# Kernel optimization log

Hardware: AMD Instinct MI355X
Metric: run time of the kernel (lower is better)

Reference implementation:

```python
import jax, jax.numpy as jnp
import numpy as np

H = 16   # heads
DK = 64  # d_model // heads
D = 1024 # d_model


def _linear_heads(x, W, b):
    # x: (bs, n, D) -> (bs, H, n, DK)
    y = x @ W.T + b
    bs, n, _ = y.shape
    return y.reshape(bs, n, H, DK).transpose(0, 2, 1, 3)


def setup_inputs() -> dict:
    key = jax.random.key(0)
    ks = jax.random.split(key, 16)
    s = 0.02
    inp = {
        "w_feat": jax.random.normal(ks[0], (4, 128, D), jnp.float32),
        "v_feat": jax.random.normal(ks[1], (4, 1024, D), jnp.float32),
        "Ww1": jax.random.normal(ks[2], (D, D), jnp.float32) * s,
        "bw1": jnp.zeros((D,), jnp.float32),
        "Wv1": jax.random.normal(ks[3], (D, D), jnp.float32) * s,
        "bv1": jnp.zeros((D,), jnp.float32),
        "Wv2": jax.random.normal(ks[4], (D, D), jnp.float32) * s,
        "bv2": jnp.zeros((D,), jnp.float32),
        "Wv3": jax.random.normal(ks[5], (D, D), jnp.float32) * s,
        "bv3": jnp.zeros((D,), jnp.float32),
        "Wv4": jax.random.normal(ks[6], (D, D), jnp.float32) * s,
        "bv4": jnp.zeros((D,), jnp.float32),
        "Wout": jax.random.normal(ks[7], (D, D), jnp.float32) * s,
        "bout": jnp.zeros((D,), jnp.float32),
    }
    return inp


def reference(w_feat, v_feat, Ww1, bw1, Wv1, bv1, Wv2, bv2, Wv3, bv3, Wv4, bv4, Wout, bout):
    bs = w_feat.shape[0]
    w1 = _linear_heads(w_feat, Ww1, bw1)  # (bs,H,n_w,DK)
    v1 = _linear_heads(v_feat, Wv1, bv1)  # (bs,H,n_v,DK)
    v2 = _linear_heads(v_feat, Wv2, bv2)
    v3 = _linear_heads(v_feat, Wv3, bv3)
    v4 = _linear_heads(v_feat, Wv4, bv4)

    # cross path: softmax over n_v of (w1 @ v3^T), summed over n_w -> (bs,H,n_v)
    cross = jax.nn.softmax(jnp.einsum('bhwd,bhvd->bhwv', w1, v3), axis=-1).sum(-2)
    # self path: v1 @ v2^T -> (bs,H,n_v,n_v), plus broadcast cross bias
    scores = jnp.einsum('bhid,bhjd->bhij', v1, v2) + cross[:, :, None, :]
    scores = jax.nn.softmax(scores, axis=-1)  # dropout is identity at eval
    ctx = jnp.einsum('bhij,bhjd->bhid', scores, v4)  # (bs,H,n_v,DK)
    concat = ctx.transpose(0, 2, 1, 3).reshape(bs, -1, D)
    return concat @ Wout.T + bout
```

## Files before the change

kernel.cpp:

```cpp
#include <hip/hip_runtime.h>

typedef __attribute__((ext_vector_type(8))) short short8;
typedef __attribute__((ext_vector_type(4))) float f32x4;

__device__ __forceinline__ unsigned short f2bf(float f) {
  unsigned int x = __float_as_uint(f);
  x += 0x7fffu + ((x >> 16) & 1u);
  return (unsigned short)(x >> 16);
}

__device__ __forceinline__ void gload_lds16(const void* g, void* l) {
  __builtin_amdgcn_global_load_lds((const __attribute__((address_space(1))) unsigned int*)g,
                                   (__attribute__((address_space(3))) unsigned int*)l, 16, 0, 0);
}

__global__ void cvt_f2b(const float* __restrict__ s, unsigned short* __restrict__ d, int n) {
  int i = (blockIdx.x * 256 + threadIdx.x) * 4;
  if (i < n) {
    float4 v = *(const float4*)(s + i);
    ushort4 o;
    o.x = f2bf(v.x); o.y = f2bf(v.y); o.z = f2bf(v.z); o.w = f2bf(v.w);
    *(ushort4*)(d + i) = o;
  }
}

__global__ void gather_bias(const float* __restrict__ b0, const float* __restrict__ b1,
                            const float* __restrict__ b2, const float* __restrict__ b3,
                            float* __restrict__ out) {
  int i = blockIdx.x * 256 + threadIdx.x;
  const float* src = (i < 1024) ? b0 : (i < 2048) ? b1 : (i < 3072) ? b2 : b3;
  out[i] = src[i & 1023];
}

__global__ void zero_f32(float* __restrict__ p, int n4) {
  int i = blockIdx.x * 256 + threadIdx.x;
  if (i < n4) *(float4*)(p + i * 4) = float4{0.f, 0.f, 0.f, 0.f};
}

template<int MODE, int BM, int BN, int WM, int WN>
__global__ __launch_bounds__(WM * WN * 64, 2) void gemm_pipe(
    const unsigned short* __restrict__ X, const unsigned short* __restrict__ Wt,
    const float* __restrict__ bias, void* __restrict__ o0, void* __restrict__ o1,
    void* __restrict__ o2, void* __restrict__ o3, int nnShift) {
  constexpr int T = WM * WN * 64;
  constexpr int WAVES = WM * WN;
  constexpr int MR = BM / WM / 16;
  constexpr int NR = BN / WN / 16;
  constexpr int MH = MR / 2;
  constexpr int AI = BM * 8 / T;
  constexpr int BI = BN * 8 / T;
  constexpr int NT = 1024 / 64;

  __shared__ unsigned short As[2][BM][64];
  __shared__ unsigned short Bs[2][BN][64];

  const int tid = threadIdx.x, lane = tid & 63, wv = tid >> 6;
  const int wm = wv % WM, wn = wv / WM;
  const int wMb = wm * (BM / WM), wNb = wn * (BN / WN);
  const int rowbase = blockIdx.x * BM, colbase = blockIdx.y * BN;
  const int rq = lane >> 4, cq = lane & 15;

  f32x4 acc[MR][NR] = {};

  auto stage = [&](int s, int kt) {
#pragma unroll
    for (int j = 0; j < AI; ++j) {
      int cb = (j * WAVES + wv) * 64;
      int row = (cb + lane) >> 3;
      int srcc = (lane & 7) ^ (row & 7);
      gload_lds16(X + (size_t)(rowbase + row) * 1024 + kt * 64 + srcc * 8,
                  &As[s][cb >> 3][0]);
    }
#pragma unroll
    for (int j = 0; j < BI; ++j) {
      int cb = (j * WAVES + wv) * 64;
      int row = (cb + lane) >> 3;
      int srcc = (lane & 7) ^ (row & 7);
      gload_lds16(Wt + (size_t)(colbase + row) * 1024 + kt * 64 + srcc * 8,
                  &Bs[s][cb >> 3][0]);
    }
  };

  auto ktile = [&](int t, bool last) {
    if (last) asm volatile("s_waitcnt vmcnt(0)" ::: "memory");
    else      asm volatile("s_waitcnt vmcnt(8)" ::: "memory");
    __builtin_amdgcn_s_barrier();
    asm volatile("" ::: "memory");
    const int s = t & 1;
    short8 bf[NR][2];
#pragma unroll
    for (int jf = 0; jf < NR; ++jf)
#pragma unroll
      for (int kk = 0; kk < 2; ++kk) {
        int row = wNb + jf * 16 + cq;
        int pc = (kk * 4 + rq) ^ (cq & 7);
        bf[jf][kk] = *(const short8*)(&Bs[s][row][pc * 8]);
      }
#pragma unroll
    for (int mh = 0; mh < 2; ++mh) {
      short8 af[MH][2];
#pragma unroll
      for (int i = 0; i < MH; ++i)
#pragma unroll
        for (int kk = 0; kk < 2; ++kk) {
          int row = wMb + (mh * MH + i) * 16 + cq;
          int pc = (kk * 4 + rq) ^ (cq & 7);
          af[i][kk] = *(const short8*)(&As[s][row][pc * 8]);
        }
      __builtin_amdgcn_s_setprio(1);
#pragma unroll
      for (int i = 0; i < MH; ++i)
#pragma unroll
        for (int jf = 0; jf < NR; ++jf)
#pragma unroll
          for (int kk = 0; kk < 2; ++kk)
            acc[mh * MH + i][jf] = __builtin_amdgcn_mfma_f32_16x16x32_bf16(
                af[i][kk], bf[jf][kk], acc[mh * MH + i][jf], 0, 0, 0);
      __builtin_amdgcn_s_setprio(0);
    }
    asm volatile("" ::: "memory");
    __builtin_amdgcn_s_barrier();
    asm volatile("" ::: "memory");
    if (t + 2 < NT) stage(s, t + 2);
  };

  stage(0, 0);
  stage(1, 1);
  for (int t = 0; t < NT - 1; ++t) ktile(t, false);
  ktile(NT - 1, true);

#pragma unroll
  for (int m = 0; m < MR; ++m)
#pragma unroll
    for (int n = 0; n < NR; ++n)
#pragma unroll
      for (int r = 0; r < 4; ++r) {
        int grow = rowbase + wMb + m * 16 + rq * 4 + r;
        int gcol = colbase + wNb + n * 16 + cq;
        float val = acc[m][n][r] + bias[gcol];
        if (MODE == 2) {
          ((float*)o0)[(size_t)grow * 1024 + gcol] = val;
        } else if (MODE == 0) {
          int bb = grow >> nnShift;
          int nr = grow & ((1 << nnShift) - 1);
          int hh = gcol >> 6, dd = gcol & 63;
          ((unsigned short*)o0)[((((size_t)bb * 16 + hh) << nnShift) + nr) * 64 + dd] = f2bf(val);
        } else {
          int which = gcol >> 10;
          int lcol = gcol & 1023;
          int bb = grow >> 10, nr = grow & 1023;
          int hh = lcol >> 6, dd = lcol & 63;
          void* op = (which == 0) ? o0 : (which == 1) ? o1 : (which == 2) ? o2 : o3;
          if (which < 3)
            ((unsigned short*)op)[((((size_t)bb * 16 + hh) << 10) + nr) * 64 + dd] = f2bf(val);
          else
            ((unsigned short*)op)[(((size_t)bb * 16 + hh) * 64 + dd) * 1024 + nr] = f2bf(val);
        }
      }
}

__global__ __launch_bounds__(256) void cross_kernel(const unsigned short* __restrict__ w1,
                                                    const unsigned short* __restrict__ v3,
                                                    float* __restrict__ cross) {
  __shared__ float cbuf[4][1024];
  const int tid = threadIdx.x, lane = tid & 63, wv = tid >> 6;
  const int rq = lane >> 4, cq = lane & 15;
  for (int i = tid; i < 4096; i += 256) ((float*)cbuf)[i] = 0.f;
  __syncthreads();
  const int bh = blockIdx.x >> 1, half = blockIdx.x & 1;
  const unsigned short* w1h = w1 + (size_t)bh * 128 * 64;
  const unsigned short* v3h = v3 + (size_t)bh * 1024 * 64;
  const int w0 = half * 64 + wv * 16;
  short8 a_w[2];
#pragma unroll
  for (int kk = 0; kk < 2; ++kk)
    a_w[kk] = *(const short8*)(w1h + (size_t)(w0 + cq) * 64 + kk * 32 + rq * 8);
  float mrow[4], lrow[4];
#pragma unroll
  for (int r = 0; r < 4; ++r) { mrow[r] = -3e38f; lrow[r] = 0.f; }
  for (int jt = 0; jt < 1024; jt += 64) {
    f32x4 s[4] = {};
#pragma unroll
    for (int n = 0; n < 4; ++n) {
      short8 bk[2];
#pragma unroll
      for (int kk = 0; kk < 2; ++kk)
        bk[kk] = *(const short8*)(v3h + (size_t)(jt + n * 16 + cq) * 64 + kk * 32 + rq * 8);
#pragma unroll
      for (int kk = 0; kk < 2; ++kk)
        s[n] = __builtin_amdgcn_mfma_f32_16x16x32_bf16(a_w[kk], bk[kk], s[n], 0, 0, 0);
    }
    float tm[4], ps[4];
#pragma unroll
    for (int r = 0; r < 4; ++r)
      tm[r] = fmaxf(fmaxf(s[0][r], s[1][r]), fmaxf(s[2][r], s[3][r]));
    for (int off = 1; off < 16; off <<= 1)
#pragma unroll
      for (int r = 0; r < 4; ++r) tm[r] = fmaxf(tm[r], __shfl_xor(tm[r], off));
#pragma unroll
    for (int r = 0; r < 4; ++r) {
      float mn = fmaxf(mrow[r], tm[r]);
      float al = __expf(mrow[r] - mn);
      mrow[r] = mn;
      float p = 0.f;
#pragma unroll
      for (int n = 0; n < 4; ++n) p += __expf(s[n][r] - mn);
      ps[r] = p;
      lrow[r] *= al;
    }
    for (int off = 1; off < 16; off <<= 1)
#pragma unroll
      for (int r = 0; r < 4; ++r) ps[r] += __shfl_xor(ps[r], off);
#pragma unroll
    for (int r = 0; r < 4; ++r) lrow[r] += ps[r];
  }
  float rl[4];
#pragma unroll
  for (int r = 0; r < 4; ++r) rl[r] = 1.f / lrow[r];
  for (int jt = 0; jt < 1024; jt += 64) {
    f32x4 s[4] = {};
#pragma unroll
    for (int n = 0; n < 4; ++n) {
      short8 bk[2];
#pragma unroll
      for (int kk = 0; kk < 2; ++kk)
        bk[kk] = *(const short8*)(v3h + (size_t)(jt + n * 16 + cq) * 64 + kk * 32 + rq * 8);
#pragma unroll
      for (int kk = 0; kk < 2; ++kk)
        s[n] = __builtin_amdgcn_mfma_f32_16x16x32_bf16(a_w[kk], bk[kk], s[n], 0, 0, 0);
    }
    float colsum[4] = {0.f, 0.f, 0.f, 0.f};
#pragma unroll
    for (int n = 0; n < 4; ++n)
#pragma unroll
      for (int r = 0; r < 4; ++r)
        colsum[n] += __expf(s[n][r] - mrow[r]) * rl[r];
#pragma unroll
    for (int n = 0; n < 4; ++n) {
      colsum[n] += __shfl_xor(colsum[n], 16);
      colsum[n] += __shfl_xor(colsum[n], 32);
    }
    if (lane < 16) {
#pragma unroll
      for (int n = 0; n < 4; ++n) cbuf[wv][jt + n * 16 + lane] += colsum[n];
    }
  }
  __syncthreads();
  for (int j = tid; j < 1024; j += 256)
    atomicAdd(&cross[(size_t)bh * 1024 + j], cbuf[0][j] + cbuf[1][j] + cbuf[2][j] + cbuf[3][j]);
}

__global__ __launch_bounds__(256) void attn_kernel(const unsigned short* __restrict__ v1,
                                                   const unsigned short* __restrict__ v2,
                                                   const unsigned short* __restrict__ v4t,
                                                   const float* __restrict__ cross,
                                                   unsigned short* __restrict__ ctx) {
  __shared__ unsigned short Kt[2][64][64];
  __shared__ unsigned short Vt[2][64][64];
  __shared__ unsigned short Pbuf[4][16][64];
  const int bid = ((blockIdx.x & 7) << 7) | (blockIdx.x >> 3);
  const int bh = bid >> 4, ib = bid & 15;
  const int b = bh >> 4, h = bh & 15;
  const int tid = threadIdx.x, lane = tid & 63, wv = tid >> 6;
  const int rq = lane >> 4, cq = lane & 15;
  const unsigned short* v1h = v1 + (size_t)bh * 1024 * 64;
  const unsigned short* v2h = v2 + (size_t)bh * 1024 * 64;
  const unsigned short* v4h = v4t + (size_t)bh * 64 * 1024;
  const float* ch = cross + (size_t)bh * 1024;
  const int i0 = ib * 64 + wv * 16;
  const int sr = lane >> 3;
  const int sc = ((lane & 7) ^ sr) * 8;
  short8 b_q[2];
#pragma unroll
  for (int kk = 0; kk < 2; ++kk)
    b_q[kk] = *(const short8*)(v1h + (size_t)(i0 + cq) * 64 + kk * 32 + rq * 8);
  float m = -3e38f, lsum = 0.f;
  f32x4 o[4] = {};

#pragma unroll
  for (int p = 0; p < 2; ++p) {
    int r = wv * 8 + p * 32 + sr;
    gload_lds16(v2h + (size_t)r * 64 + sc, &Kt[0][wv * 8 + p * 32][0]);
    gload_lds16(v4h + (size_t)r * 1024 + sc, &Vt[0][wv * 8 + p * 32][0]);
  }
  __syncthreads();

  for (int t = 0; t < 16; ++t) {
    const int cur = t & 1;
    const int jt = t * 64;
    if (t < 15) {
#pragma unroll
      for (int p = 0; p < 2; ++p) {
        int r = wv * 8 + p * 32 + sr;
        gload_lds16(v2h + (size_t)(jt + 64 + r) * 64 + sc, &Kt[cur ^ 1][wv * 8 + p * 32][0]);
        gload_lds16(v4h + (size_t)r * 1024 + jt + 64 + sc, &Vt[cur ^ 1][wv * 8 + p * 32][0]);
      }
    }
    f32x4 s[4] = {};
#pragma unroll
    for (int mp = 0; mp < 4; ++mp) {
      const int row = mp * 16 + cq;
      const char* base = (const char*)&Kt[cur][row][0];
#pragma unroll
      for (int kk = 0; kk < 2; ++kk) {
        short8 ak = *(const short8*)(base + ((((kk << 2) | rq) ^ (cq & 7)) << 4));
        s[mp] = __builtin_amdgcn_mfma_f32_16x16x32_bf16(ak, b_q[kk], s[mp], 0, 0, 0);
      }
    }
#pragma unroll
    for (int mp = 0; mp < 4; ++mp) {
      float4 cj = *(const float4*)(ch + jt + mp * 16 + rq * 4);
      s[mp][0] += cj.x; s[mp][1] += cj.y; s[mp][2] += cj.z; s[mp][3] += cj.w;
    }
    float tm = s[0][0];
#pragma unroll
    for (int mp = 0; mp < 4; ++mp)
#pragma unroll
      for (int r = 0; r < 4; ++r) tm = fmaxf(tm, s[mp][r]);
    tm = fmaxf(tm, __shfl_xor(tm, 16));
    tm = fmaxf(tm, __shfl_xor(tm, 32));
    float mn = fmaxf(m, tm);
    float alpha = __expf(m - mn);
    m = mn;
    float ps = 0.f;
#pragma unroll
    for (int mp = 0; mp < 4; ++mp)
#pragma unroll
      for (int r = 0; r < 4; ++r) {
        float p = __expf(s[mp][r] - mn);
        s[mp][r] = p;
        ps += p;
      }
    ps += __shfl_xor(ps, 16);
    ps += __shfl_xor(ps, 32);
    lsum = lsum * alpha + ps;
    {
      char* pb = (char*)&Pbuf[wv][cq][0];
      const int sw = (cq & 7) << 4;
#pragma unroll
      for (int mp = 0; mp < 4; ++mp) {
        ushort4 pw;
        pw.x = f2bf(s[mp][0]); pw.y = f2bf(s[mp][1]);
        pw.z = f2bf(s[mp][2]); pw.w = f2bf(s[mp][3]);
        *(ushort4*)(pb + ((mp * 32 + rq * 8) ^ sw)) = pw;
      }
    }
    short8 a_p[2];
    {
      const char* pb = (const char*)&Pbuf[wv][cq][0];
      const int sw = (cq & 7) << 4;
#pragma unroll
      for (int kk = 0; kk < 2; ++kk)
        a_p[kk] = *(const short8*)(pb + ((kk * 64 + rq * 16) ^ sw));
    }
    float al[4];
#pragma unroll
    for (int r = 0; r < 4; ++r) al[r] = __shfl(alpha, rq * 4 + r);
#pragma unroll
    for (int n = 0; n < 4; ++n)
#pragma unroll
      for (int r = 0; r < 4; ++r) o[n][r] *= al[r];
#pragma unroll
    for (int n = 0; n < 4; ++n) {
      const int row = n * 16 + cq;
      const char* base = (const char*)&Vt[cur][row][0];
#pragma unroll
      for (int kk = 0; kk < 2; ++kk) {
        short8 bv = *(const short8*)(base + ((((kk << 2) | rq) ^ (cq & 7)) << 4));
        o[n] = __builtin_amdgcn_mfma_f32_16x16x32_bf16(a_p[kk], bv, o[n], 0, 0, 0);
      }
    }
    __syncthreads();
  }
  float li[4];
#pragma unroll
  for (int r = 0; r < 4; ++r) li[r] = __shfl(lsum, rq * 4 + r);
#pragma unroll
  for (int n = 0; n < 4; ++n)
#pragma unroll
    for (int r = 0; r < 4; ++r) {
      float val = o[n][r] / li[r];
      int row = i0 + rq * 4 + r;
      int col = h * 64 + n * 16 + cq;
      ctx[((size_t)b * 1024 + row) * 1024 + col] = f2bf(val);
    }
}

extern "C" void kernel_launch(void* const* d_in, const int* in_sizes, int n_in,
                              void* d_out, int out_size, void* d_ws, size_t ws_size,
                              hipStream_t stream) {
  const int bs = in_sizes[0] / (128 * 1024);
  char* w = (char*)d_ws;
  size_t off = 0;
  auto alloc = [&](size_t bytes) -> void* {
    void* p = w + off;
    off += (bytes + 255) & ~(size_t)255;
    return p;
  };
  unsigned short* wfeat_b = (unsigned short*)alloc((size_t)bs * 128 * 1024 * 2);
  unsigned short* vfeat_b = (unsigned short*)alloc((size_t)bs * 1024 * 1024 * 2);
  unsigned short* Ww1b = (unsigned short*)alloc((size_t)1024 * 1024 * 2);
  unsigned short* Wv1b = (unsigned short*)alloc((size_t)1024 * 1024 * 2);
  unsigned short* Wv2b = (unsigned short*)alloc((size_t)1024 * 1024 * 2);
  unsigned short* Wv3b = (unsigned short*)alloc((size_t)1024 * 1024 * 2);
  unsigned short* Wv4b = (unsigned short*)alloc((size_t)1024 * 1024 * 2);
  unsigned short* Woutb = (unsigned short*)alloc((size_t)1024 * 1024 * 2);
  unsigned short* w1b = (unsigned short*)alloc((size_t)bs * 16 * 128 * 64 * 2);
  unsigned short* v1b = (unsigned short*)alloc((size_t)bs * 16 * 1024 * 64 * 2);
  unsigned short* v2b = (unsigned short*)alloc((size_t)bs * 16 * 1024 * 64 * 2);
  unsigned short* v3b = (unsigned short*)alloc((size_t)bs * 16 * 1024 * 64 * 2);
  unsigned short* v4tb = (unsigned short*)alloc((size_t)bs * 16 * 64 * 1024 * 2);
  unsigned short* ctxb = (unsigned short*)alloc((size_t)bs * 1024 * 1024 * 2);
  float* crossb = (float*)alloc((size_t)bs * 16 * 1024 * 4);
  float* biascat = (float*)alloc((size_t)4096 * 4);

  auto cvt = [&](const void* src, unsigned short* dst, int n) {
    cvt_f2b<<<(n / 4 + 255) / 256, 256, 0, stream>>>((const float*)src, dst, n);
  };
  cvt(d_in[0], wfeat_b, bs * 128 * 1024);
  cvt(d_in[1], vfeat_b, bs * 1024 * 1024);
  cvt(d_in[2], Ww1b, 1024 * 1024);
  cvt(d_in[4], Wv1b, 1024 * 1024);
  cvt(d_in[6], Wv2b, 1024 * 1024);
  cvt(d_in[8], Wv3b, 1024 * 1024);
  cvt(d_in[10], Wv4b, 1024 * 1024);
  cvt(d_in[12], Woutb, 1024 * 1024);
  gather_bias<<<16, 256, 0, stream>>>((const float*)d_in[5], (const float*)d_in[7],
                                      (const float*)d_in[9], (const float*)d_in[11], biascat);
  zero_f32<<<64, 256, 0, stream>>>(crossb, bs * 16 * 1024 / 4);

  gemm_pipe<0, 128, 128, 2, 2><<<dim3(4, 8), 256, 0, stream>>>(
      wfeat_b, Ww1b, (const float*)d_in[3], w1b, nullptr, nullptr, nullptr, 7);
  gemm_pipe<3, 256, 256, 2, 4><<<dim3(16, 16), 512, 0, stream>>>(
      vfeat_b, Wv1b, biascat, v1b, v2b, v3b, v4tb, 10);
  cross_kernel<<<bs * 16 * 2, 256, 0, stream>>>(w1b, v3b, crossb);
  attn_kernel<<<bs * 16 * 16, 256, 0, stream>>>(v1b, v2b, v4tb, crossb, ctxb);
  gemm_pipe<2, 128, 128, 2, 2><<<dim3(32, 8), 256, 0, stream>>>(
      ctxb, Woutb, (const float*)d_in[13], (float*)d_out, nullptr, nullptr, nullptr, 0);
}
```

Before: 308.3 us.

## Merge fp32-to-bf16 conversions into one launch and retile projection GEMMs

Replaces the eight per-tensor conversion launches with a single kernel that looks up its source and destination segment from a cumulative offset table, cutting launch overhead. The fused V projection GEMM moves from 256x256 tiles with 512 threads to 128x128 tiles with 256 threads over a 32x32 grid. The output GEMM moves to 64x128 tiles for more blocks. The GEMM template is generalized so smaller tiles work: the vmcnt wait count now follows loads per stage, and the M-half split handles MR=1. Smaller tiles raise occupancy and CU coverage but lower per-block data reuse.

```diff
diff --git a/kernel.cpp b/kernel.cpp
--- a/kernel.cpp
+++ b/kernel.cpp
@@ -14,14 +14,22 @@
                                    (__attribute__((address_space(3))) unsigned int*)l, 16, 0, 0);
 }
 
-__global__ void cvt_f2b(const float* __restrict__ s, unsigned short* __restrict__ d, int n) {
-  int i = (blockIdx.x * 256 + threadIdx.x) * 4;
-  if (i < n) {
-    float4 v = *(const float4*)(s + i);
-    ushort4 o;
-    o.x = f2bf(v.x); o.y = f2bf(v.y); o.z = f2bf(v.z); o.w = f2bf(v.w);
-    *(ushort4*)(d + i) = o;
-  }
+struct CvtArgs {
+  const float* src[8];
+  unsigned short* dst[8];
+  int cum4[9];
+};
+__global__ void cvt_all(CvtArgs a, int total4) {
+  int g = blockIdx.x * 256 + threadIdx.x;
+  if (g >= total4) return;
+  int s = 0;
+#pragma unroll
+  for (int k = 1; k < 8; ++k) s += (g >= a.cum4[k]);
+  int off = g - a.cum4[s];
+  float4 v = *(const float4*)(a.src[s] + (size_t)off * 4);
+  ushort4 o;
+  o.x = f2bf(v.x); o.y = f2bf(v.y); o.z = f2bf(v.z); o.w = f2bf(v.w);
+  *(ushort4*)(a.dst[s] + (size_t)off * 4) = o;
 }
 
 __global__ void gather_bias(const float* __restrict__ b0, const float* __restrict__ b1,
@@ -46,7 +54,8 @@
   constexpr int WAVES = WM * WN;
   constexpr int MR = BM / WM / 16;
   constexpr int NR = BN / WN / 16;
-  constexpr int MH = MR / 2;
+  constexpr int MH = (MR > 1) ? MR / 2 : 1;
+  constexpr int MHALVES = MR / MH;
   constexpr int AI = BM * 8 / T;
   constexpr int BI = BN * 8 / T;
   constexpr int NT = 1024 / 64;
@@ -82,8 +91,13 @@
   };
 
   auto ktile = [&](int t, bool last) {
-    if (last) asm volatile("s_waitcnt vmcnt(0)" ::: "memory");
-    else      asm volatile("s_waitcnt vmcnt(8)" ::: "memory");
+    if (last) {
+      asm volatile("s_waitcnt vmcnt(0)" ::: "memory");
+    } else {
+      if constexpr (AI + BI == 8)      asm volatile("s_waitcnt vmcnt(8)" ::: "memory");
+      else if constexpr (AI + BI == 6) asm volatile("s_waitcnt vmcnt(6)" ::: "memory");
+      else                             asm volatile("s_waitcnt vmcnt(0)" ::: "memory");
+    }
     __builtin_amdgcn_s_barrier();
     asm volatile("" ::: "memory");
     const int s = t & 1;
@@ -97,7 +111,7 @@
         bf[jf][kk] = *(const short8*)(&Bs[s][row][pc * 8]);
       }
 #pragma unroll
-    for (int mh = 0; mh < 2; ++mh) {
+    for (int mh = 0; mh < MHALVES; ++mh) {
       short8 af[MH][2];
 #pragma unroll
       for (int i = 0; i < MH; ++i)
@@ -414,27 +428,28 @@
   float* crossb = (float*)alloc((size_t)bs * 16 * 1024 * 4);
   float* biascat = (float*)alloc((size_t)4096 * 4);
 
-  auto cvt = [&](const void* src, unsigned short* dst, int n) {
-    cvt_f2b<<<(n / 4 + 255) / 256, 256, 0, stream>>>((const float*)src, dst, n);
-  };
-  cvt(d_in[0], wfeat_b, bs * 128 * 1024);
-  cvt(d_in[1], vfeat_b, bs * 1024 * 1024);
-  cvt(d_in[2], Ww1b, 1024 * 1024);
-  cvt(d_in[4], Wv1b, 1024 * 1024);
-  cvt(d_in[6], Wv2b, 1024 * 1024);
-  cvt(d_in[8], Wv3b, 1024 * 1024);
-  cvt(d_in[10], Wv4b, 1024 * 1024);
-  cvt(d_in[12], Woutb, 1024 * 1024);
+  CvtArgs ca;
+  const int srcIdx[8] = {0, 1, 2, 4, 6, 8, 10, 12};
+  unsigned short* dsts[8] = {wfeat_b, vfeat_b, Ww1b, Wv1b, Wv2b, Wv3b, Wv4b, Woutb};
+  int cum = 0;
+  for (int k = 0; k < 8; ++k) {
+    ca.src[k] = (const float*)d_in[srcIdx[k]];
+    ca.dst[k] = dsts[k];
+    ca.cum4[k] = cum;
+    cum += in_sizes[srcIdx[k]] / 4;
+  }
+  ca.cum4[8] = cum;
+  cvt_all<<<(cum + 255) / 256, 256, 0, stream>>>(ca, cum);
   gather_bias<<<16, 256, 0, stream>>>((const float*)d_in[5], (const float*)d_in[7],
                                       (const float*)d_in[9], (const float*)d_in[11], biascat);
   zero_f32<<<64, 256, 0, stream>>>(crossb, bs * 16 * 1024 / 4);
 
   gemm_pipe<0, 128, 128, 2, 2><<<dim3(4, 8), 256, 0, stream>>>(
       wfeat_b, Ww1b, (const float*)d_in[3], w1b, nullptr, nullptr, nullptr, 7);
-  gemm_pipe<3, 256, 256, 2, 4><<<dim3(16, 16), 512, 0, stream>>>(
+  gemm_pipe<3, 128, 128, 2, 2><<<dim3(32, 32), 256, 0, stream>>>(
       vfeat_b, Wv1b, biascat, v1b, v2b, v3b, v4tb, 10);
   cross_kernel<<<bs * 16 * 2, 256, 0, stream>>>(w1b, v3b, crossb);
   attn_kernel<<<bs * 16 * 16, 256, 0, stream>>>(v1b, v2b, v4tb, crossb, ctxb);
-  gemm_pipe<2, 128, 128, 2, 2><<<dim3(32, 8), 256, 0, stream>>>(
+  gemm_pipe<2, 64, 128, 2, 2><<<dim3(64, 8), 256, 0, stream>>>(
       ctxb, Woutb, (const float*)d_in[13], (float*)d_out, nullptr, nullptr, nullptr, 0);
 }
```

After: 277.8 us. -9.9%, faster.
